# Kernel optimization log

Hardware: AMD Instinct MI355X
Metric: run time of the kernel (lower is better)

## Reference

```python
import jax, jax.numpy as jnp
import numpy as np

B, N, M = 4, 10000, 10000
P = 128          # num_pts (sampled query points)
K_SAMPLE = 32    # knn_for_sample
K_SCORE = 4      # knn_for_score
Z = 128          # feature dim
SIGMA = 0.01


def setup_inputs() -> dict:
    key = jax.random.key(0)
    ks = jax.random.split(key, 16)
    rn = lambda k, shape, scale: (jax.random.normal(k, shape, dtype=jnp.float32) * scale)
    inp = {
        "noisy_pc": rn(ks[0], (B, N, 3), 1.0),
        "clean_pc": rn(ks[1], (B, M, 3), 1.0),
        "sampled_idx": jax.random.randint(ks[2], (P,), 0, N, dtype=jnp.int32),
        "Wf1": rn(ks[3], (3, 64), 1.0 / np.sqrt(3)),
        "bf1": jnp.zeros((64,), jnp.float32),
        "Wf2": rn(ks[4], (64, Z), 1.0 / np.sqrt(64)),
        "bf2": jnp.zeros((Z,), jnp.float32),
        "Ws1": rn(ks[5], (3 + Z, 128), 1.0 / np.sqrt(3 + Z)),
        "bs1": jnp.zeros((128,), jnp.float32),
        "Ws2": rn(ks[6], (128, 64), 1.0 / np.sqrt(128)),
        "bs2": jnp.zeros((64,), jnp.float32),
        "Ws3": rn(ks[7], (64, 3), 1.0 / np.sqrt(64)),
        "bs3": jnp.zeros((3,), jnp.float32),
    }
    return inp


def _sqdist(q, r):
    # q: (..., Q, 3), r: (..., R, 3) -> (..., Q, R) squared distances
    q2 = jnp.sum(q * q, axis=-1)[..., :, None]
    r2 = jnp.sum(r * r, axis=-1)[..., None, :]
    return q2 + r2 - 2.0 * jnp.matmul(q, jnp.swapaxes(r, -1, -2))


def _knn_gather(q, ref, k):
    # q: (..., Q, 3), ref: (B, R, 3) broadcast-compatible -> nn points (..., Q, k, 3)
    d = _sqdist(q, ref)
    _, idx = jax.lax.top_k(-d, k)          # nearest k (ascending distance)
    return idx


def _forward(noisy_pc, clean_pc, sampled_idx,
             Wf1, bf1, Wf2, bf2, Ws1, bs1, Ws2, bs2, Ws3, bs3):
    # f_origin: sampled query points (B, P, 3)
    f_origin = noisy_pc[:, sampled_idx, :]

    # FeatureExtraction: pointwise MLP over all N points, gather at samples
    feat = jnp.maximum(noisy_pc @ Wf1 + bf1, 0.0) @ Wf2 + bf2      # (B, N, Z)
    noisy_feat = feat[:, sampled_idx, :]                           # (B, P, Z)

    # kNN #1: for each sampled point, K_SAMPLE nearest neighbors in noisy_pc
    idx1 = _knn_gather(f_origin, noisy_pc, K_SAMPLE)               # (B, P, K_SAMPLE)
    f = jax.vmap(lambda pc, i: pc[i])(noisy_pc, idx1)              # (B, P, K_SAMPLE, 3)

    # ScoreNetwork: per-neighbor MLP on [offset, feature]
    x = f - f_origin[:, :, None, :]                                # (B, P, K_SAMPLE, 3)
    z = jnp.broadcast_to(noisy_feat[:, :, None, :], (B, P, K_SAMPLE, Z))
    h = jnp.concatenate([x, z], axis=-1)                           # (B, P, K_SAMPLE, 3+Z)
    h = jnp.maximum(h @ Ws1 + bs1, 0.0)
    h = jnp.maximum(h @ Ws2 + bs2, 0.0)
    estim_score = h @ Ws3 + bs3                                    # (B, P, K_SAMPLE, 3)

    # kNN #2: each neighbor point vs full clean cloud (the hot, huge cdist)
    # dist tensor (B, P, K_SAMPLE, M) computed without materializing the
    # repeated merge_f_origin of the original torch code.
    dot = jnp.einsum("bpkd,bmd->bpkm", f, clean_pc)
    d2 = (jnp.sum(f * f, axis=-1)[..., None]
          + jnp.sum(clean_pc * clean_pc, axis=-1)[:, None, None, :]
          - 2.0 * dot)                                             # (B, P, K_SAMPLE, M)
    _, idx2 = jax.lax.top_k(-d2, K_SCORE)                          # (B, P, K_SAMPLE, K_SCORE)
    nn = jax.vmap(lambda pc, i: pc[i])(clean_pc, idx2)             # (B, P, K_SAMPLE, K_SCORE, 3)

    ground_score = jnp.mean(nn - f[:, :, :, None, :], axis=3)      # (B, P, K_SAMPLE, 3)

    loss = 0.5 * jnp.mean(jnp.sum((estim_score - ground_score) ** 2 * (1.0 / SIGMA), axis=-1))
    return loss


def reference(noisy_pc, clean_pc, sampled_idx,
              Wf1, bf1, Wf2, bf2, Ws1, bs1, Ws2, bs2, Ws3, bs3):
    return _forward(noisy_pc, clean_pc, sampled_idx,
                    Wf1, bf1, Wf2, bf2, Ws1, bs1, Ws2, bs2, Ws3, bs3)
```

## Files before the change

### kernel.cpp

```cpp
#include <hip/hip_runtime.h>

#define BB 4
#define NN 10000
#define MM 10000
#define PP 128
#define KS 32
#define KSC 4
#define ZZ 128

#define OFF_PN 0
#define OFF_PC (OFF_PN + BB*NN*4)
#define OFF_FO (OFF_PC + BB*MM*4)
#define OFF_ZP (OFF_FO + BB*PP*4)
#define OFF_FP (OFF_ZP + BB*PP*ZZ)
#define OFF_GS (OFF_FP + BB*PP*KS*4)
#define OFF_AC (OFF_GS + BB*PP*KS*4)

#define FINF 1e30f

__global__ void k_pack(const float* __restrict__ noisy, const float* __restrict__ clean,
                       float* __restrict__ ws) {
    int t = blockIdx.x * blockDim.x + threadIdx.x;
    if (t == 0) ws[OFF_AC] = 0.0f;
    const int total = BB*NN + BB*MM;
    if (t >= total) return;
    if (t < BB*NN) {
        float x = noisy[t*3+0], y = noisy[t*3+1], z = noisy[t*3+2];
        float w = (x*x + y*y) + z*z;
        ((float4*)(ws + OFF_PN))[t] = make_float4(x, y, z, w);
    } else {
        int u = t - BB*NN;
        float x = clean[u*3+0], y = clean[u*3+1], z = clean[u*3+2];
        float w = -0.5f * ((x*x + y*y) + z*z);
        ((float4*)(ws + OFF_PC))[u] = make_float4(x, y, z, w);
    }
}

__global__ void k_feat(const int* __restrict__ sidx,
                       const float* __restrict__ Wf1, const float* __restrict__ bf1,
                       const float* __restrict__ Wf2, const float* __restrict__ bf2,
                       const float* __restrict__ Ws1, const float* __restrict__ bs1,
                       float* __restrict__ ws) {
    int wave = (blockIdx.x * blockDim.x + threadIdx.x) >> 6;
    int lane = threadIdx.x & 63;
    if (wave >= BB*PP) return;
    int b = wave / PP, p = wave % PP;
    int si = sidx[p];
    float4 q = ((const float4*)(ws + OFF_PN))[b*NN + si];
    if (lane == 0) ((float4*)(ws + OFF_FO))[wave] = q;
    float h = bf1[lane];
    h = fmaf(q.x, Wf1[0*64 + lane], h);
    h = fmaf(q.y, Wf1[1*64 + lane], h);
    h = fmaf(q.z, Wf1[2*64 + lane], h);
    h = fmaxf(h, 0.0f);
    float fa = bf2[lane], fb = bf2[64 + lane];
    for (int i = 0; i < 64; ++i) {
        float hi = __shfl(h, i);
        fa = fmaf(hi, Wf2[i*ZZ + lane],      fa);
        fb = fmaf(hi, Wf2[i*ZZ + 64 + lane], fb);
    }
    float za = bs1[lane], zb = bs1[64 + lane];
    for (int i = 0; i < 64; ++i) {
        float va = __shfl(fa, i);
        float vb = __shfl(fb, i);
        za = fmaf(va, Ws1[(3 + i)*128 + lane],       za);
        zb = fmaf(va, Ws1[(3 + i)*128 + 64 + lane],  zb);
        za = fmaf(vb, Ws1[(67 + i)*128 + lane],      za);
        zb = fmaf(vb, Ws1[(67 + i)*128 + 64 + lane], zb);
    }
    ws[OFF_ZP + wave*ZZ + lane]      = za;
    ws[OFF_ZP + wave*ZZ + 64 + lane] = zb;
}

#define CAP1 512
__global__ __launch_bounds__(256) void k_knn1(const int* __restrict__ sidx, float* __restrict__ ws) {
    __shared__ float cd[CAP1];
    __shared__ int   ci[CAP1];
    __shared__ float wtau[4];
    __shared__ int   cnt;
    int blk = blockIdx.x;
    int b = blk >> 7, p = blk & 127;
    int tid = threadIdx.x;
    int w = tid >> 6, lane = tid & 63;
    const float4* pts = ((const float4*)(ws + OFF_PN)) + b*NN;
    float4 q = pts[sidx[p]];
    if (tid == 0) cnt = 0;
    float t0 = FINF, t1 = FINF;
    for (int j = tid; j < NN; j += 256) {
        float4 r = pts[j];
        float dot = fmaf(q.z, r.z, fmaf(q.y, r.y, q.x*r.x));
        float d = fmaf(dot, -2.0f, q.w + r.w);
        t1 = fminf(t1, fmaxf(t0, d));
        t0 = fminf(t0, d);
    }
    float m = 0.0f;
    for (int r = 0; r < KS; ++r) {
        m = t0;
        m = fminf(m, __shfl_xor(m, 1));
        m = fminf(m, __shfl_xor(m, 2));
        m = fminf(m, __shfl_xor(m, 4));
        m = fminf(m, __shfl_xor(m, 8));
        m = fminf(m, __shfl_xor(m, 16));
        m = fminf(m, __shfl_xor(m, 32));
        if (t0 == m) { t0 = t1; t1 = FINF; }
    }
    if (lane == 0) wtau[w] = m;
    __syncthreads();
    float tau = fminf(fminf(wtau[0], wtau[1]), fminf(wtau[2], wtau[3]));
    for (int j = tid; j < NN; j += 256) {
        float4 r = pts[j];
        float dot = fmaf(q.z, r.z, fmaf(q.y, r.y, q.x*r.x));
        float d = fmaf(dot, -2.0f, q.w + r.w);
        if (d <= tau) {
            int pos = atomicAdd(&cnt, 1);
            if (pos < CAP1) { cd[pos] = d; ci[pos] = j; }
        }
    }
    __syncthreads();
    int C = cnt; if (C > CAP1) C = CAP1;
    for (int i = tid; i < C; i += 256) {
        float di = cd[i]; int ii = ci[i];
        int rank = 0;
        for (int j2 = 0; j2 < C; ++j2) {
            float dj = cd[j2]; int ij = ci[j2];
            rank += ((dj < di) || (dj == di && ij < ii)) ? 1 : 0;
        }
        if (rank < KS) ((float4*)(ws + OFF_FP))[blk*KS + rank] = pts[ii];
    }
}

#define CHK2 2000
#define QPB 32

#define KDECL(c) \
    float fxv##c, fyv##c, fzv##c, tauv##c; \
    float te0##c=-FINF, te1##c=-FINF, te2##c=-FINF, te3##c=-FINF; \
    int   ti0##c=-1,   ti1##c=-1,   ti2##c=-1,   ti3##c=-1; \
    float ta0##c=-FINF, ta1##c=-FINF;

#define KLOAD(c) { float4 f4_ = ((const float4*)(ws + OFF_FP))[qbase + qg*4 + c]; \
    fxv##c = f4_.x; fyv##c = f4_.y; fzv##c = f4_.z; }

#define AUPD(c, R) { float e_ = fmaf(fzv##c,(R).z,fmaf(fyv##c,(R).y,fmaf(fxv##c,(R).x,(R).w))); \
    ta1##c = fmaxf(ta1##c, fminf(ta0##c, e_)); ta0##c = fmaxf(ta0##c, e_); }

#define AMRG(c) { \
    float h0_ = ta0##c, h1_ = ta1##c; \
    _Pragma("unroll") \
    for (int r_ = 0; r_ < 4; ++r_) { \
        float m_ = h0_; \
        m_ = fmaxf(m_, __shfl_xor(m_, 1)); \
        m_ = fmaxf(m_, __shfl_xor(m_, 2)); \
        m_ = fmaxf(m_, __shfl_xor(m_, 4)); \
        if (h0_ == m_) { h0_ = h1_; h1_ = -FINF; } \
        if (sub == r_) sWA[qg*4 + c][w*4 + r_] = m_; \
    } }

#define EVC(c, R) float ev##c = fmaf(fzv##c,(R).z,fmaf(fyv##c,(R).y,fmaf(fxv##c,(R).x,(R).w)));

#define INSC(c, JV) { \
    if (ev##c >= tauv##c && ev##c > te3##c) { \
        if (ev##c > te1##c) { \
            te3##c = te2##c; ti3##c = ti2##c; te2##c = te1##c; ti2##c = ti1##c; \
            if (ev##c > te0##c) { te1##c = te0##c; ti1##c = ti0##c; te0##c = ev##c; ti0##c = (JV); } \
            else                { te1##c = ev##c; ti1##c = (JV); } \
        } else if (ev##c > te2##c) { te3##c = te2##c; ti3##c = ti2##c; te2##c = ev##c; ti2##c = (JV); } \
        else                       { te3##c = ev##c; ti3##c = (JV); } \
    } }

#define BSCAN(BUF, BASE) \
    for (int t_ = 0; t_ < 63; ++t_) { \
        if (t_ < 62 || sub < 4) { \
            int loc_ = sbase + t_*8 + sub; \
            float4 r_ = sp[BUF][loc_]; \
            EVC(0, r_) EVC(1, r_) EVC(2, r_) EVC(3, r_) \
            float mx_ = fmaxf(fmaxf(ev0, ev1), fmaxf(ev2, ev3)); \
            if (mx_ >= cmin) { \
                int gj_ = (BASE) + loc_; \
                INSC(0, gj_) INSC(1, gj_) INSC(2, gj_) INSC(3, gj_) \
            } \
        } }

#define BMRG(c) { \
    _Pragma("unroll") \
    for (int r_ = 0; r_ < 4; ++r_) { \
        float bk_ = te0##c; int bi_ = ti0##c; int bl_ = lane; \
        _Pragma("unroll") \
        for (int off_ = 1; off_ < 8; off_ <<= 1) { \
            float ok_ = __shfl_xor(bk_, off_); \
            int   oi_ = __shfl_xor(bi_, off_); \
            int   ol_ = __shfl_xor(bl_, off_); \
            if (ok_ > bk_ || (ok_ == bk_ && oi_ < bi_)) { bk_ = ok_; bi_ = oi_; bl_ = ol_; } \
        } \
        if (sub == r_) { sME[qg*4 + c][w*4 + r_] = bk_; sMI[qg*4 + c][w*4 + r_] = bi_; } \
        if (lane == bl_) { te0##c = te1##c; ti0##c = ti1##c; te1##c = te2##c; ti1##c = ti2##c; \
                           te2##c = te3##c; ti2##c = ti3##c; te3##c = -FINF; ti3##c = -1; } \
    } }

#define STAGE(BUF, CHUNK) \
    for (int u_ = tid; u_ < CHK2; u_ += 256) sp[BUF][u_] = pts[(CHUNK)*CHK2 + u_];

__global__ __launch_bounds__(256) void k_knn2(float* __restrict__ ws) {
    __shared__ float4 sp[2][CHK2];
    __shared__ float  sWA[QPB][16];
    __shared__ float  sME[QPB][16];
    __shared__ int    sMI[QPB][16];
    __shared__ float  sTau[QPB];
    int tid  = threadIdx.x;
    int w    = tid >> 6;
    int lane = tid & 63;
    int sub  = lane & 7;
    int qg   = lane >> 3;
    int qbase = blockIdx.x * QPB;
    int b = qbase >> 12;
    int sbase = w * 500;
    const float4* pts = ((const float4*)(ws + OFF_PC)) + b*MM;

    KDECL(0) KDECL(1) KDECL(2) KDECL(3)
    KLOAD(0) KLOAD(1) KLOAD(2) KLOAD(3)

    STAGE(0, 0)
    __syncthreads();
    STAGE(1, 1)

    for (int t_ = 0; t_ < 63; ++t_) {
        if (t_ < 62 || sub < 4) {
            float4 r_ = sp[0][sbase + t_*8 + sub];
            AUPD(0, r_) AUPD(1, r_) AUPD(2, r_) AUPD(3, r_)
        }
    }
    AMRG(0) AMRG(1) AMRG(2) AMRG(3)
    __syncthreads();
    if (tid < QPB) {
        float b0=-FINF, b1=-FINF, b2=-FINF, b3=-FINF;
        #pragma unroll
        for (int u = 0; u < 16; ++u) {
            float v = sWA[tid][u];
            b3 = fmaxf(b3, fminf(b2, v));
            b2 = fmaxf(b2, fminf(b1, v));
            b1 = fmaxf(b1, fminf(b0, v));
            b0 = fmaxf(b0, v);
        }
        sTau[tid] = b3;
    }
    __syncthreads();
    tauv0 = sTau[qg*4 + 0]; tauv1 = sTau[qg*4 + 1];
    tauv2 = sTau[qg*4 + 2]; tauv3 = sTau[qg*4 + 3];
    float cmin = fminf(fminf(tauv0, tauv1), fminf(tauv2, tauv3));

    BSCAN(0, 0)
    __syncthreads();
    STAGE(0, 2) BSCAN(1, CHK2)
    __syncthreads();
    STAGE(1, 3) BSCAN(0, 2*CHK2)
    __syncthreads();
    STAGE(0, 4) BSCAN(1, 3*CHK2)
    __syncthreads();
    BSCAN(0, 4*CHK2)

    BMRG(0) BMRG(1) BMRG(2) BMRG(3)
    __syncthreads();
    if (tid < QPB) {
        int q = qbase + tid;
        float4 f4 = ((const float4*)(ws + OFF_FP))[q];
        float b0=-FINF, b1=-FINF, b2=-FINF, b3=-FINF;
        int   j0=-1,   j1=-1,   j2=-1,   j3=-1;
        #pragma unroll
        for (int u = 0; u < 16; ++u) {
            float e = sME[tid][u]; int ii = sMI[tid][u];
            bool l3 = (e > b3) || (e == b3 && ii < j3);
            if (l3) {
                bool l2 = (e > b2) || (e == b2 && ii < j2);
                if (l2) {
                    b3 = b2; j3 = j2;
                    bool l1 = (e > b1) || (e == b1 && ii < j1);
                    if (l1) {
                        b2 = b1; j2 = j1;
                        bool l0 = (e > b0) || (e == b0 && ii < j0);
                        if (l0) { b1 = b0; j1 = j0; b0 = e; j0 = ii; }
                        else    { b1 = e; j1 = ii; }
                    } else { b2 = e; j2 = ii; }
                } else { b3 = e; j3 = ii; }
            }
        }
        float4 n0 = pts[j0], n1 = pts[j1], n2 = pts[j2], n3 = pts[j3];
        float gx = 0.f, gy = 0.f, gz = 0.f;
        gx += n0.x - f4.x; gy += n0.y - f4.y; gz += n0.z - f4.z;
        gx += n1.x - f4.x; gy += n1.y - f4.y; gz += n1.z - f4.z;
        gx += n2.x - f4.x; gy += n2.y - f4.y; gz += n2.z - f4.z;
        gx += n3.x - f4.x; gy += n3.y - f4.y; gz += n3.z - f4.z;
        float* gsp = ws + OFF_GS + (size_t)q*4;
        gsp[0] = gx*0.25f; gsp[1] = gy*0.25f; gsp[2] = gz*0.25f;
    }
}

__global__ __launch_bounds__(256) void k_mlp(const float* __restrict__ Ws1,
                                             const float* __restrict__ Ws2, const float* __restrict__ bs2,
                                             const float* __restrict__ Ws3, const float* __restrict__ bs3,
                                             float* __restrict__ ws) {
    __shared__ float4 sG[2][128];
    __shared__ float4 sW2[128][16];
    __shared__ float  sB2[64];
    __shared__ float  sW3[64][3];
    __shared__ float  sB3[3];
    __shared__ float  sE[3][4][64];
    int tid = threadIdx.x;
    int w = tid >> 6, lane = tid & 63;
    for (int u = tid; u < 2048; u += 256) ((float4*)sW2)[u] = ((const float4*)Ws2)[u];
    if (tid < 64) sB2[tid] = bs2[tid];
    if (tid < 192) ((float*)sW3)[tid] = Ws3[tid];
    if (tid < 3) sB3[tid] = bs3[tid];
    {
        int grp = tid >> 7, i = tid & 127;
        sG[grp][i] = make_float4(ws[OFF_ZP + (blockIdx.x*2 + grp)*ZZ + i],
                                 Ws1[i], Ws1[128 + i], Ws1[256 + i]);
    }
    __syncthreads();

    int g = blockIdx.x*64 + lane;
    float4 f4 = ((const float4*)(ws + OFF_FP))[g];
    float4 fo = ((const float4*)(ws + OFF_FO))[g >> 5];
    float x0 = f4.x - fo.x, x1 = f4.y - fo.y, x2 = f4.z - fo.z;
    int grp = lane >> 5;

    float4 a[4];
    #pragma unroll
    for (int qq = 0; qq < 4; ++qq) a[qq] = make_float4(0.f, 0.f, 0.f, 0.f);
    for (int i = 0; i < 128; ++i) {
        float4 gv = sG[grp][i];
        float h1 = fmaf(x2, gv.w, fmaf(x1, gv.z, fmaf(x0, gv.y, gv.x)));
        h1 = fmaxf(h1, 0.0f);
        #pragma unroll
        for (int qq = 0; qq < 4; ++qq) {
            float4 wv = sW2[i][w*4 + qq];
            a[qq].x = fmaf(h1, wv.x, a[qq].x);
            a[qq].y = fmaf(h1, wv.y, a[qq].y);
            a[qq].z = fmaf(h1, wv.z, a[qq].z);
            a[qq].w = fmaf(h1, wv.w, a[qq].w);
        }
    }
    float p0 = 0.f, p1 = 0.f, p2 = 0.f;
    #pragma unroll
    for (int qq = 0; qq < 4; ++qq) {
        float av[4] = {a[qq].x, a[qq].y, a[qq].z, a[qq].w};
        #pragma unroll
        for (int cc = 0; cc < 4; ++cc) {
            int j = w*16 + qq*4 + cc;
            float h2 = fmaxf(av[cc] + sB2[j], 0.0f);
            p0 = fmaf(h2, sW3[j][0], p0);
            p1 = fmaf(h2, sW3[j][1], p1);
            p2 = fmaf(h2, sW3[j][2], p2);
        }
    }
    sE[0][w][lane] = p0; sE[1][w][lane] = p1; sE[2][w][lane] = p2;
    __syncthreads();
    if (w == 0) {
        float ee0 = ((sE[0][0][lane] + sE[0][1][lane]) + sE[0][2][lane]) + sE[0][3][lane] + sB3[0];
        float ee1 = ((sE[1][0][lane] + sE[1][1][lane]) + sE[1][2][lane]) + sE[1][3][lane] + sB3[1];
        float ee2 = ((sE[2][0][lane] + sE[2][1][lane]) + sE[2][2][lane]) + sE[2][3][lane] + sB3[2];
        const float* gsp = ws + OFF_GS + (size_t)g*4;
        float d0 = ee0 - gsp[0], d1 = ee1 - gsp[1], d2 = ee2 - gsp[2];
        float t = ((d0*d0 + d1*d1) + d2*d2) * 100.0f;
        for (int off = 32; off > 0; off >>= 1) t += __shfl_down(t, off);
        if (lane == 0) atomicAdd(ws + OFF_AC, t);
    }
}

__global__ void k_fin(const float* __restrict__ ws, float* __restrict__ out) {
    if (threadIdx.x == 0 && blockIdx.x == 0)
        out[0] = ws[OFF_AC] * (1.0f / 32768.0f);
}

extern "C" void kernel_launch(void* const* d_in, const int* in_sizes, int n_in,
                              void* d_out, int out_size, void* d_ws, size_t ws_size,
                              hipStream_t stream) {
    const float* noisy = (const float*)d_in[0];
    const float* clean = (const float*)d_in[1];
    const int*   sidx  = (const int*)  d_in[2];
    const float* Wf1 = (const float*)d_in[3];
    const float* bf1 = (const float*)d_in[4];
    const float* Wf2 = (const float*)d_in[5];
    const float* bf2 = (const float*)d_in[6];
    const float* Ws1 = (const float*)d_in[7];
    const float* bs1 = (const float*)d_in[8];
    const float* Ws2 = (const float*)d_in[9];
    const float* bs2 = (const float*)d_in[10];
    const float* Ws3 = (const float*)d_in[11];
    const float* bs3 = (const float*)d_in[12];
    float* ws  = (float*)d_ws;
    float* out = (float*)d_out;

    k_pack<<<(BB*NN + BB*MM + 255)/256, 256, 0, stream>>>(noisy, clean, ws);
    k_feat<<<(BB*PP*64)/256, 256, 0, stream>>>(sidx, Wf1, bf1, Wf2, bf2, Ws1, bs1, ws);
    k_knn1<<<BB*PP, 256, 0, stream>>>(sidx, ws);
    k_knn2<<<(BB*PP*KS)/QPB, 256, 0, stream>>>(ws);
    k_mlp<<<(BB*PP*KS)/64, 256, 0, stream>>>(Ws1, Ws2, bs2, Ws3, bs3, ws);
    k_fin<<<1, 64, 0, stream>>>(ws, out);
}
```

Before: 230.1 us.

## Replace per-thread top-4 insertion with shared candidate append and rank select in knn2

The second kNN kernel now uses 512 threads and 1000-point staging chunks. The per-lane register top-4 insertion lists and the shuffle-based merge are replaced. Every point that passes the threshold is appended with a shared-memory atomic into a per-query candidate buffer (cap 128). The top 4 are then chosen by a parallel rank count. The threshold is estimated from the first 2000 points across 8 waves, and the aim is to cut branchy register insertion and raise parallelism per block. Results could be wrong if more than 128 candidates pass the threshold for a query, and contention on the shared atomics adds cost.

```diff
diff --git a/kernel.cpp b/kernel.cpp
--- a/kernel.cpp
+++ b/kernel.cpp
@@ -129,20 +129,26 @@
     }
 }
 
-#define CHK2 2000
+#define CHK2 1000
+#define NCH2 10
 #define QPB 32
-
-#define KDECL(c) \
-    float fxv##c, fyv##c, fzv##c, tauv##c; \
-    float te0##c=-FINF, te1##c=-FINF, te2##c=-FINF, te3##c=-FINF; \
-    int   ti0##c=-1,   ti1##c=-1,   ti2##c=-1,   ti3##c=-1; \
-    float ta0##c=-FINF, ta1##c=-FINF;
-
-#define KLOAD(c) { float4 f4_ = ((const float4*)(ws + OFF_FP))[qbase + qg*4 + c]; \
+#define CAP2 128
+
+#define K2Q(c) float fxv##c, fyv##c, fzv##c, tauv##c; \
+    float ta0##c = -FINF, ta1##c = -FINF;
+
+#define K2LOAD(c) { float4 f4_ = ((const float4*)(ws + OFF_FP))[qbase + qg*4 + c]; \
     fxv##c = f4_.x; fyv##c = f4_.y; fzv##c = f4_.z; }
 
 #define AUPD(c, R) { float e_ = fmaf(fzv##c,(R).z,fmaf(fyv##c,(R).y,fmaf(fxv##c,(R).x,(R).w))); \
     ta1##c = fmaxf(ta1##c, fminf(ta0##c, e_)); ta0##c = fmaxf(ta0##c, e_); }
+
+#define ASCAN(BUF) \
+    for (int t_ = 0; t_ < 16; ++t_) { \
+        if (t_ < 15 || sub < 5) { \
+            float4 r_ = sp[BUF][sbase + t_*8 + sub]; \
+            AUPD(0, r_) AUPD(1, r_) AUPD(2, r_) AUPD(3, r_) \
+        } }
 
 #define AMRG(c) { \
     float h0_ = ta0##c, h1_ = ta1##c; \
@@ -158,54 +164,34 @@
 
 #define EVC(c, R) float ev##c = fmaf(fzv##c,(R).z,fmaf(fyv##c,(R).y,fmaf(fxv##c,(R).x,(R).w)));
 
-#define INSC(c, JV) { \
-    if (ev##c >= tauv##c && ev##c > te3##c) { \
-        if (ev##c > te1##c) { \
-            te3##c = te2##c; ti3##c = ti2##c; te2##c = te1##c; ti2##c = ti1##c; \
-            if (ev##c > te0##c) { te1##c = te0##c; ti1##c = ti0##c; te0##c = ev##c; ti0##c = (JV); } \
-            else                { te1##c = ev##c; ti1##c = (JV); } \
-        } else if (ev##c > te2##c) { te3##c = te2##c; ti3##c = ti2##c; te2##c = ev##c; ti2##c = (JV); } \
-        else                       { te3##c = ev##c; ti3##c = (JV); } \
-    } }
+#define APP(c) if (ev##c >= tauv##c) { \
+    int pos_ = atomicAdd(&sCnt[qg*4 + c], 1); \
+    if (pos_ < CAP2) { sCE[qg*4 + c][pos_] = ev##c; sCI[qg*4 + c][pos_] = gj_; } }
 
 #define BSCAN(BUF, BASE) \
-    for (int t_ = 0; t_ < 63; ++t_) { \
-        if (t_ < 62 || sub < 4) { \
+    for (int t_ = 0; t_ < 16; ++t_) { \
+        if (t_ < 15 || sub < 5) { \
             int loc_ = sbase + t_*8 + sub; \
             float4 r_ = sp[BUF][loc_]; \
             EVC(0, r_) EVC(1, r_) EVC(2, r_) EVC(3, r_) \
             float mx_ = fmaxf(fmaxf(ev0, ev1), fmaxf(ev2, ev3)); \
             if (mx_ >= cmin) { \
                 int gj_ = (BASE) + loc_; \
-                INSC(0, gj_) INSC(1, gj_) INSC(2, gj_) INSC(3, gj_) \
+                APP(0) APP(1) APP(2) APP(3) \
             } \
         } }
 
-#define BMRG(c) { \
-    _Pragma("unroll") \
-    for (int r_ = 0; r_ < 4; ++r_) { \
-        float bk_ = te0##c; int bi_ = ti0##c; int bl_ = lane; \
-        _Pragma("unroll") \
-        for (int off_ = 1; off_ < 8; off_ <<= 1) { \
-            float ok_ = __shfl_xor(bk_, off_); \
-            int   oi_ = __shfl_xor(bi_, off_); \
-            int   ol_ = __shfl_xor(bl_, off_); \
-            if (ok_ > bk_ || (ok_ == bk_ && oi_ < bi_)) { bk_ = ok_; bi_ = oi_; bl_ = ol_; } \
-        } \
-        if (sub == r_) { sME[qg*4 + c][w*4 + r_] = bk_; sMI[qg*4 + c][w*4 + r_] = bi_; } \
-        if (lane == bl_) { te0##c = te1##c; ti0##c = ti1##c; te1##c = te2##c; ti1##c = ti2##c; \
-                           te2##c = te3##c; ti2##c = ti3##c; te3##c = -FINF; ti3##c = -1; } \
-    } }
-
 #define STAGE(BUF, CHUNK) \
-    for (int u_ = tid; u_ < CHK2; u_ += 256) sp[BUF][u_] = pts[(CHUNK)*CHK2 + u_];
-
-__global__ __launch_bounds__(256) void k_knn2(float* __restrict__ ws) {
+    for (int u_ = tid; u_ < CHK2; u_ += 512) sp[BUF][u_] = pts[(CHUNK)*CHK2 + u_];
+
+__global__ __launch_bounds__(512) void k_knn2(float* __restrict__ ws) {
     __shared__ float4 sp[2][CHK2];
-    __shared__ float  sWA[QPB][16];
-    __shared__ float  sME[QPB][16];
-    __shared__ int    sMI[QPB][16];
+    __shared__ float  sWA[QPB][33];
+    __shared__ float  sCE[QPB][CAP2 + 1];
+    __shared__ int    sCI[QPB][CAP2 + 1];
     __shared__ float  sTau[QPB];
+    __shared__ int    sCnt[QPB];
+    __shared__ int    sTop[QPB][4];
     int tid  = threadIdx.x;
     int w    = tid >> 6;
     int lane = tid & 63;
@@ -213,28 +199,26 @@
     int qg   = lane >> 3;
     int qbase = blockIdx.x * QPB;
     int b = qbase >> 12;
-    int sbase = w * 500;
+    int sbase = w * 125;
     const float4* pts = ((const float4*)(ws + OFF_PC)) + b*MM;
 
-    KDECL(0) KDECL(1) KDECL(2) KDECL(3)
-    KLOAD(0) KLOAD(1) KLOAD(2) KLOAD(3)
+    K2Q(0) K2Q(1) K2Q(2) K2Q(3)
+    K2LOAD(0) K2LOAD(1) K2LOAD(2) K2LOAD(3)
+    if (tid < QPB) sCnt[tid] = 0;
 
     STAGE(0, 0)
     __syncthreads();
     STAGE(1, 1)
 
-    for (int t_ = 0; t_ < 63; ++t_) {
-        if (t_ < 62 || sub < 4) {
-            float4 r_ = sp[0][sbase + t_*8 + sub];
-            AUPD(0, r_) AUPD(1, r_) AUPD(2, r_) AUPD(3, r_)
-        }
-    }
+    ASCAN(0)
+    __syncthreads();
+    ASCAN(1)
     AMRG(0) AMRG(1) AMRG(2) AMRG(3)
     __syncthreads();
     if (tid < QPB) {
-        float b0=-FINF, b1=-FINF, b2=-FINF, b3=-FINF;
+        float b0 = -FINF, b1 = -FINF, b2 = -FINF, b3 = -FINF;
         #pragma unroll
-        for (int u = 0; u < 16; ++u) {
+        for (int u = 0; u < 32; ++u) {
             float v = sWA[tid][u];
             b3 = fmaxf(b3, fminf(b2, v));
             b2 = fmaxf(b2, fminf(b1, v));
@@ -250,40 +234,45 @@
 
     BSCAN(0, 0)
     __syncthreads();
-    STAGE(0, 2) BSCAN(1, CHK2)
+    STAGE(0, 2) BSCAN(1, 1*CHK2)
     __syncthreads();
     STAGE(1, 3) BSCAN(0, 2*CHK2)
     __syncthreads();
     STAGE(0, 4) BSCAN(1, 3*CHK2)
     __syncthreads();
-    BSCAN(0, 4*CHK2)
-
-    BMRG(0) BMRG(1) BMRG(2) BMRG(3)
+    STAGE(1, 5) BSCAN(0, 4*CHK2)
+    __syncthreads();
+    STAGE(0, 6) BSCAN(1, 5*CHK2)
+    __syncthreads();
+    STAGE(1, 7) BSCAN(0, 6*CHK2)
+    __syncthreads();
+    STAGE(0, 8) BSCAN(1, 7*CHK2)
+    __syncthreads();
+    STAGE(1, 9) BSCAN(0, 8*CHK2)
+    __syncthreads();
+    BSCAN(1, 9*CHK2)
+    __syncthreads();
+
+    {
+        int qi = tid >> 4;
+        int sl = tid & 15;
+        int C = sCnt[qi]; if (C > CAP2) C = CAP2;
+        for (int i = sl; i < C; i += 16) {
+            float ei = sCE[qi][i]; int ii = sCI[qi][i];
+            int rank = 0;
+            for (int j = 0; j < C; ++j) {
+                float ej = sCE[qi][j]; int ij = sCI[qi][j];
+                rank += ((ej > ei) || (ej == ei && ij < ii)) ? 1 : 0;
+            }
+            if (rank < KSC) sTop[qi][rank] = ii;
+        }
+    }
     __syncthreads();
     if (tid < QPB) {
         int q = qbase + tid;
         float4 f4 = ((const float4*)(ws + OFF_FP))[q];
-        float b0=-FINF, b1=-FINF, b2=-FINF, b3=-FINF;
-        int   j0=-1,   j1=-1,   j2=-1,   j3=-1;
-        #pragma unroll
-        for (int u = 0; u < 16; ++u) {
-            float e = sME[tid][u]; int ii = sMI[tid][u];
-            bool l3 = (e > b3) || (e == b3 && ii < j3);
-            if (l3) {
-                bool l2 = (e > b2) || (e == b2 && ii < j2);
-                if (l2) {
-                    b3 = b2; j3 = j2;
-                    bool l1 = (e > b1) || (e == b1 && ii < j1);
-                    if (l1) {
-                        b2 = b1; j2 = j1;
-                        bool l0 = (e > b0) || (e == b0 && ii < j0);
-                        if (l0) { b1 = b0; j1 = j0; b0 = e; j0 = ii; }
-                        else    { b1 = e; j1 = ii; }
-                    } else { b2 = e; j2 = ii; }
-                } else { b3 = e; j3 = ii; }
-            }
-        }
-        float4 n0 = pts[j0], n1 = pts[j1], n2 = pts[j2], n3 = pts[j3];
+        float4 n0 = pts[sTop[tid][0]], n1 = pts[sTop[tid][1]];
+        float4 n2 = pts[sTop[tid][2]], n3 = pts[sTop[tid][3]];
         float gx = 0.f, gy = 0.f, gz = 0.f;
         gx += n0.x - f4.x; gy += n0.y - f4.y; gz += n0.z - f4.z;
         gx += n1.x - f4.x; gy += n1.y - f4.y; gz += n1.z - f4.z;
@@ -393,7 +382,7 @@
     k_pack<<<(BB*NN + BB*MM + 255)/256, 256, 0, stream>>>(noisy, clean, ws);
     k_feat<<<(BB*PP*64)/256, 256, 0, stream>>>(sidx, Wf1, bf1, Wf2, bf2, Ws1, bs1, ws);
     k_knn1<<<BB*PP, 256, 0, stream>>>(sidx, ws);
-    k_knn2<<<(BB*PP*KS)/QPB, 256, 0, stream>>>(ws);
+    k_knn2<<<(BB*PP*KS)/QPB, 512, 0, stream>>>(ws);
     k_mlp<<<(BB*PP*KS)/64, 256, 0, stream>>>(Ws1, Ws2, bs2, Ws3, bs3, ws);
     k_fin<<<1, 64, 0, stream>>>(ws, out);
 }
```

Measured after the change: 220.9 us. -4.0%, faster.
